# Kernel optimization log

Hardware: AMD Instinct MI355X
Metric: run time of the kernel (lower is better)

## Reference

```python
import jax, jax.numpy as jnp
import numpy as np

DIM = 384
NH = 16
HD = DIM // NH          # 24
HID = DIM * 4           # titan/cms hidden
RD = 2 * (HD // 3 // 2) # 8 rope channels per axis (d/h/w), 3*RD == HD


def _ln(x, scale, bias):
    m = x.mean(-1, keepdims=True)
    v = ((x - m) ** 2).mean(-1, keepdims=True)
    return (x - m) * jax.lax.rsqrt(v + 1e-5) * scale + bias


def _mlp(x, w1, b1, w2, b2):
    # TitanMemory / CMS level: Linear -> GELU -> Linear (titan_layers=2)
    h = jax.nn.gelu(x @ w1 + b1, approximate=False)
    return h @ w2 + b2


def _rotate(x, pos):
    # rotate_queries_or_keys: interleaved rotary. x: [B,nh,N,d], pos: [N]
    d = x.shape[-1]
    inv_freq = 1.0 / (10000.0 ** (jnp.arange(0, d, 2, dtype=jnp.float32) / d))
    ang = pos[:, None] * inv_freq[None, :]              # [N, d/2]
    sin, cos = jnp.sin(ang), jnp.cos(ang)
    x1, x2 = x[..., 0::2], x[..., 1::2]
    y1 = x1 * cos - x2 * sin
    y2 = x1 * sin + x2 * cos
    return jnp.stack([y1, y2], axis=-1).reshape(x.shape)


def _rope3d(q, T, H, W):
    # 3D RoPE on frame tokens (action_tokens=0): time / height / width axes
    B, N, D = q.shape
    qh = q.reshape(B, N, NH, HD).transpose(0, 2, 1, 3)   # [B,nh,N,hd]
    ids = jnp.arange(T * H * W)
    tpos = (ids // (H * W)).astype(jnp.float32)
    hpos = ((ids % (H * W)) // W).astype(jnp.float32)
    wpos = (ids % W).astype(jnp.float32)
    qd = _rotate(qh[..., :RD], tpos)
    qhh = _rotate(qh[..., RD:2 * RD], hpos)
    qww = _rotate(qh[..., 2 * RD:3 * RD], wpos)
    out = jnp.concatenate([qd, qhh, qww], axis=-1)
    return out.transpose(0, 2, 1, 3).reshape(B, N, D)


def setup_inputs() -> dict:
    key = jax.random.key(0)
    ks = jax.random.split(key, 8)
    B, T, H, W = 8, 8, 16, 16
    N = T * H * W
    p = lambda k, sh: jax.random.normal(k, sh, jnp.float32) * 0.02
    return {
        "x": jax.random.normal(ks[0], (B, N, DIM), jnp.float32),
        "norm1_scale": jnp.ones((DIM,), jnp.float32),
        "norm1_bias": jnp.zeros((DIM,), jnp.float32),
        "norm2_scale": jnp.ones((DIM,), jnp.float32),
        "norm2_bias": jnp.zeros((DIM,), jnp.float32),
        "q_w": p(ks[1], (DIM, DIM)),
        # stacked Titan memories: [M_k, M_v, M_eta, M_alpha, M_memory]
        "titan_w1": p(ks[2], (5, DIM, HID)),
        "titan_b1": jnp.zeros((5, HID), jnp.float32),
        "titan_w2": p(ks[3], (5, HID, DIM)),
        "titan_b2": jnp.zeros((5, DIM), jnp.float32),
        "out_w": p(ks[4], (DIM, DIM)),
        "out_b": jnp.zeros((DIM,), jnp.float32),
        # CMS levels: [fast, medium, slow]
        "cms_w1": p(ks[5], (3, DIM, HID)),
        "cms_b1": jnp.zeros((3, HID), jnp.float32),
        "cms_w2": p(ks[6], (3, HID, DIM)),
        "cms_b2": jnp.zeros((3, DIM), jnp.float32),
        "T": T, "H": H, "W": W, "action_tokens": 0,
    }


def reference(x, norm1_scale, norm1_bias, norm2_scale, norm2_bias, q_w,
              titan_w1, titan_b1, titan_w2, titan_b2, out_w, out_b,
              cms_w1, cms_b1, cms_w2, cms_b2, T, H, W, action_tokens):
    # Phase A: self-modifying Titan (eval path: retrieval only)
    y = _ln(x, norm1_scale, norm1_bias)
    q = y @ q_w                                  # static query projection (Eq. 76)
    q = _rope3d(q, T, H, W)                      # 3D RoPE (action_tokens == 0)
    out = _mlp(q, titan_w1[4], titan_b1[4], titan_w2[4], titan_b2[4])  # M_memory(q)
    out = out @ out_w + out_b                    # out_proj
    x = x + out                                  # residual (drop_path = identity)
    # Phase B: CMS multi-frequency MLP cascade
    y = _ln(x, norm2_scale, norm2_bias)
    cms = sum(_mlp(y, cms_w1[i], cms_b1[i], cms_w2[i], cms_b2[i]) for i in range(3))
    return x + cms
```

## Files before the change

kernel.cpp:

```cpp
#include <hip/hip_runtime.h>
#include <math.h>

typedef unsigned short u16;
typedef unsigned int u32;
typedef __attribute__((ext_vector_type(8))) short short8;
typedef __attribute__((ext_vector_type(4))) float f32x4;

#define DIM 384
#define HID 1536

static __device__ __forceinline__ float bf2f(u32 b){ return __uint_as_float(b << 16); }
static __device__ __forceinline__ u16 f2bf(float f){
  u32 u = __float_as_uint(f);
  u32 r = (u + 0x7fffu + ((u >> 16) & 1u)) >> 16;
  return (u16)r;
}
static __device__ __forceinline__ float gelu_fast(float v){
  float u = v * fmaf(0.0713548162726f, v * v, 1.59576912161f);
  float e = exp2f(-1.44269504089f * u);
  return v * __builtin_amdgcn_rcpf(1.0f + e);
}
static __device__ __forceinline__ void gload_lds16(const u16* g, u16* l){
  __builtin_amdgcn_global_load_lds(
      (__attribute__((address_space(1))) void*)(void*)const_cast<u16*>(g),
      (__attribute__((address_space(3))) void*)(void*)l, 16, 0, 0);
}

__global__ __launch_bounds__(256) void ln_kernel(const float* __restrict__ x,
    const float* __restrict__ sc, const float* __restrict__ bi, u16* __restrict__ y){
  int lane = threadIdx.x & 63;
  int row = blockIdx.x * 4 + (threadIdx.x >> 6);
  const float* xr = x + (size_t)row * DIM;
  float v[6];
  float s = 0.f, sq = 0.f;
#pragma unroll
  for (int i = 0; i < 6; ++i){
    float f = xr[lane + 64*i];
    v[i] = f; s += f; sq += f*f;
  }
#pragma unroll
  for (int o = 1; o < 64; o <<= 1){ s += __shfl_xor(s, o); sq += __shfl_xor(sq, o); }
  float mean = s * (1.0f/DIM);
  float var = sq * (1.0f/DIM) - mean*mean;
  float inv = rsqrtf(var + 1e-5f);
  u16* yr = y + (size_t)row * DIM;
#pragma unroll
  for (int i = 0; i < 6; ++i){
    int c = lane + 64*i;
    yr[c] = f2bf((v[i] - mean) * inv * sc[c] + bi[c]);
  }
}

__global__ __launch_bounds__(256) void rope_kernel(u16* __restrict__ q,
    const int* __restrict__ Tp, const int* __restrict__ Hp, const int* __restrict__ Wp,
    int Mtok){
  int idx = blockIdx.x * 256 + threadIdx.x;
  int tok = idx / 192;
  if (tok >= Mtok) return;
  int p = idx - tok * 192;
  int H = *Hp, W = *Wp, T = *Tp;
  int HW = H * W;
  int Ns = T * HW;
  int n = tok % Ns;
  int head = p / 12;
  int pp = p - head * 12;
  int s = pp >> 2, f = pp & 3;
  float pos;
  if (s == 0)      pos = (float)(n / HW);
  else if (s == 1) pos = (float)((n / W) % H);
  else             pos = (float)(n % W);
  const float LOG2_10000 = 13.28771237954945f;
  float inv = exp2f(-0.25f * (float)f * LOG2_10000);
  float ang = pos * inv;
  float sn = sinf(ang), cs = cosf(ang);
  size_t base = (size_t)tok * DIM + head * 24 + s * 8 + 2 * f;
  u32 u = *(u32*)(q + base);
  float x1 = bf2f(u & 0xffffu), x2 = bf2f(u >> 16);
  float y1 = x1 * cs - x2 * sn;
  float y2 = x1 * sn + x2 * cs;
  *(u32*)(q + base) = (u32)f2bf(y1) | ((u32)f2bf(y2) << 16);
}

template<int R, int C>
__global__ __launch_bounds__(256) void transpose_kernel(
    const float* __restrict__ s0, const float* __restrict__ s1,
    const float* __restrict__ s2, const float* __restrict__ s3,
    u16* __restrict__ d0, u16* __restrict__ d1, u16* __restrict__ d2, u16* __restrict__ d3,
    int dstStride){
  const float* src = (blockIdx.z == 0) ? s0 : (blockIdx.z == 1) ? s1 : (blockIdx.z == 2) ? s2 : s3;
  u16* dst         = (blockIdx.z == 0) ? d0 : (blockIdx.z == 1) ? d1 : (blockIdx.z == 2) ? d2 : d3;
  __shared__ u16 t[32][33];
  int tx = threadIdx.x & 31, ty = threadIdx.x >> 5;
  int r0 = blockIdx.y * 32, c0 = blockIdx.x * 32;
#pragma unroll
  for (int i = 0; i < 4; ++i)
    t[ty + 8*i][tx] = f2bf(src[(size_t)(r0 + ty + 8*i) * C + c0 + tx]);
  __syncthreads();
#pragma unroll
  for (int i = 0; i < 4; ++i)
    dst[(size_t)(c0 + ty + 8*i) * dstStride + r0 + tx] = t[tx][ty + 8*i];
}

__global__ void bias3_kernel(const float* __restrict__ b, float* __restrict__ o){
  int n = threadIdx.x;
  o[n] = b[n] + b[384 + n] + b[768 + n];
}

enum { E_NONE = 0, E_BIAS = 1, E_BIAS_GELU = 2, E_RES_F32 = 3, E_ACC_F32 = 4, E_FINAL = 5 };

template<int BM, int N, int K, int EPI>
__global__ __launch_bounds__(256) void gemm_kernel(
    const u16* __restrict__ A, const u16* __restrict__ Bt,
    void* __restrict__ Cv, const float* __restrict__ bias,
    const float* __restrict__ res, float* __restrict__ accbuf){
  constexpr int BN = 128, BK = 64;
  constexpr int MT = BM / 32, NT = 4;
  constexpr int AIT = BM / 32, BIT = 4;
  __shared__ __align__(16) u16 As[BM * BK];
  __shared__ __align__(16) u16 Bs[BN * BK];
  const int tid = threadIdx.x;
  const int lane = tid & 63;
  const int wv = tid >> 6;
  const int wm = (wv >> 1) * (BM / 2);
  const int wn = (wv & 1) * 64;
  const int quad = lane >> 4;
  const int l16 = lane & 15;
  const int rsw = l16 & 7;
  const size_t m0 = (size_t)blockIdx.x * BM;
  const int n0 = blockIdx.y * BN;
  const int srow = lane >> 3;
  const int scol = ((lane & 7) ^ srow) * 8;

  f32x4 acc[MT][NT];
  const f32x4 zero = {0.f, 0.f, 0.f, 0.f};
#pragma unroll
  for (int mt = 0; mt < MT; ++mt)
#pragma unroll
    for (int nt = 0; nt < NT; ++nt) acc[mt][nt] = zero;

  for (int kt = 0; kt < K; kt += BK){
#pragma unroll
    for (int i = 0; i < AIT; ++i){
      int seg = i * 4 + wv;
      gload_lds16(A + (m0 + (size_t)(seg * 8 + srow)) * K + kt + scol, As + seg * 512);
    }
#pragma unroll
    for (int i = 0; i < BIT; ++i){
      int seg = i * 4 + wv;
      gload_lds16(Bt + (size_t)(n0 + seg * 8 + srow) * K + kt + scol, Bs + seg * 512);
    }
    __syncthreads();
#pragma unroll
    for (int kk = 0; kk < 2; ++kk){
      short8 af[MT], bfr[NT];
#pragma unroll
      for (int mt = 0; mt < MT; ++mt)
        af[mt] = *(const short8*)(As + (wm + mt*16 + l16) * BK + (((kk*4 + quad) ^ rsw) << 3));
#pragma unroll
      for (int nt = 0; nt < NT; ++nt)
        bfr[nt] = *(const short8*)(Bs + (wn + nt*16 + l16) * BK + (((kk*4 + quad) ^ rsw) << 3));
#pragma unroll
      for (int mt = 0; mt < MT; ++mt)
#pragma unroll
        for (int nt = 0; nt < NT; ++nt)
          acc[mt][nt] = __builtin_amdgcn_mfma_f32_16x16x32_bf16(af[mt], bfr[nt], acc[mt][nt], 0, 0, 0);
    }
    __syncthreads();
  }

#pragma unroll
  for (int mt = 0; mt < MT; ++mt){
#pragma unroll
    for (int nt = 0; nt < NT; ++nt){
      int ncol = n0 + wn + nt*16 + l16;
      float bv = (EPI != E_NONE) ? bias[ncol] : 0.f;
      size_t mbase = m0 + wm + mt*16 + quad*4;
#pragma unroll
      for (int r = 0; r < 4; ++r){
        size_t off = (mbase + r) * N + ncol;
        float vv = acc[mt][nt][r];
        if      (EPI == E_NONE)      ((u16*)Cv)[off] = f2bf(vv);
        else if (EPI == E_BIAS)      ((u16*)Cv)[off] = f2bf(vv + bv);
        else if (EPI == E_BIAS_GELU) ((u16*)Cv)[off] = f2bf(gelu_fast(vv + bv));
        else if (EPI == E_RES_F32)   accbuf[off] = vv + bv + res[off];
        else if (EPI == E_ACC_F32)   accbuf[off] += vv + bv;
        else            ((float*)Cv)[off] = accbuf[off] + vv + bv;
      }
    }
  }
}

extern "C" void kernel_launch(void* const* d_in, const int* in_sizes, int n_in,
                              void* d_out, int out_size, void* d_ws, size_t ws_size,
                              hipStream_t stream) {
  const int W11 = DIM * HID;
  const float* x   = (const float*)d_in[0];
  const float* n1s = (const float*)d_in[1];
  const float* n1b = (const float*)d_in[2];
  const float* n2s = (const float*)d_in[3];
  const float* n2b = (const float*)d_in[4];
  const float* qw  = (const float*)d_in[5];
  const float* tw1 = (const float*)d_in[6] + 4 * W11;
  const float* tb1 = (const float*)d_in[7] + 4 * HID;
  const float* tw2 = (const float*)d_in[8] + 4 * W11;
  const float* tb2 = (const float*)d_in[9] + 4 * DIM;
  const float* ow  = (const float*)d_in[10];
  const float* ob  = (const float*)d_in[11];
  const float* cw1 = (const float*)d_in[12];
  const float* cb1 = (const float*)d_in[13];
  const float* cw2 = (const float*)d_in[14];
  const float* cb2 = (const float*)d_in[15];
  const int* Tp = (const int*)d_in[16];
  const int* Hp = (const int*)d_in[17];
  const int* Wp = (const int*)d_in[18];
  const int M = in_sizes[0] / DIM;
  const bool fused = (ws_size >= 198772224u);

  char* ws = (char*)d_ws;
  u16 *y, *h, *qwT, *owT, *w1T, *w2T, *cw1T, *cw2T;
  float *x2, *cb2s = nullptr;
  u16* qb = (u16*)d_out;
  if (fused){
    y    = (u16*) (ws + 0);
    h    = (u16*) (ws + 12582912);
    x2   = (float*)(ws + 163577856);
    qwT  = (u16*) (ws + 188743680);
    owT  = (u16*) (ws + 189038592);
    w1T  = (u16*) (ws + 189333504);
    w2T  = (u16*) (ws + 190513152);
    cw1T = (u16*) (ws + 191692800);
    cw2T = (u16*) (ws + 195231744);
    cb2s = (float*)(ws + 198770688);
  } else {
    if (ws_size < 98107392u) return;
    y    = (u16*) (ws + 0);
    h    = (u16*) (ws + 12582912);
    x2   = (float*)(ws + 62914560);
    qwT  = (u16*) (ws + 88080384);
    owT  = (u16*) (ws + 88375296);
    w1T  = (u16*) (ws + 88670208);
    w2T  = (u16*) (ws + 89849856);
    cw1T = (u16*) (ws + 91029504);
    cw2T = (u16*) (ws + 94568448);
  }

  transpose_kernel<384,384><<<dim3(12,12,2),256,0,stream>>>(
      qw, ow, qw, qw, qwT, owT, qwT, qwT, 384);
  transpose_kernel<384,1536><<<dim3(48,12,4),256,0,stream>>>(
      tw1, cw1, cw1 + W11, cw1 + 2*W11, w1T, cw1T, cw1T + W11, cw1T + 2*W11, 384);
  if (fused){
    transpose_kernel<1536,384><<<dim3(12,48,1),256,0,stream>>>(
        tw2, tw2, tw2, tw2, w2T, w2T, w2T, w2T, 1536);
    transpose_kernel<1536,384><<<dim3(12,48,3),256,0,stream>>>(
        cw2, cw2 + W11, cw2 + 2*W11, cw2, cw2T, cw2T + 1536, cw2T + 3072, cw2T, 4608);
    bias3_kernel<<<1,384,0,stream>>>(cb2, cb2s);
  } else {
    transpose_kernel<1536,384><<<dim3(12,48,4),256,0,stream>>>(
        tw2, cw2, cw2 + W11, cw2 + 2*W11, w2T, cw2T, cw2T + W11, cw2T + 2*W11, 1536);
  }

  ln_kernel<<<M/4,256,0,stream>>>(x, n1s, n1b, y);
  gemm_kernel<64,384,384,E_NONE><<<dim3(M/64,3),256,0,stream>>>(y, qwT, qb, nullptr, nullptr, nullptr);
  rope_kernel<<<(M*192)/256,256,0,stream>>>(qb, Tp, Hp, Wp, M);
  gemm_kernel<128,1536,384,E_BIAS_GELU><<<dim3(M/128,12),256,0,stream>>>(qb, w1T, h, tb1, nullptr, nullptr);
  gemm_kernel<64,384,1536,E_BIAS><<<dim3(M/64,3),256,0,stream>>>(h, w2T, qb, tb2, nullptr, nullptr);
  gemm_kernel<64,384,384,E_RES_F32><<<dim3(M/64,3),256,0,stream>>>(qb, owT, nullptr, ob, x, x2);
  ln_kernel<<<M/4,256,0,stream>>>(x2, n2s, n2b, y);
  if (fused){
    gemm_kernel<128,4608,384,E_BIAS_GELU><<<dim3(M/128,36),256,0,stream>>>(
        y, cw1T, h, cb1, nullptr, nullptr);
    gemm_kernel<64,384,4608,E_FINAL><<<dim3(M/64,3),256,0,stream>>>(
        h, cw2T, d_out, cb2s, nullptr, x2);
  } else {
    for (int i = 0; i < 3; ++i){
      gemm_kernel<128,1536,384,E_BIAS_GELU><<<dim3(M/128,12),256,0,stream>>>(
          y, cw1T + i*W11, h, cb1 + i*HID, nullptr, nullptr);
      if (i < 2)
        gemm_kernel<64,384,1536,E_ACC_F32><<<dim3(M/64,3),256,0,stream>>>(
            h, cw2T + i*W11, nullptr, cb2 + i*DIM, nullptr, x2);
      else
        gemm_kernel<64,384,1536,E_FINAL><<<dim3(M/64,3),256,0,stream>>>(
            h, cw2T + i*W11, d_out, cb2 + i*DIM, nullptr, x2);
    }
  }
}
```

Measured before the change: 434.3 us.

## Fuse MLP up-projection, GELU and down-projection into one LDS-resident kernel

Adds a fused MLP kernel in which each 64-row block keeps its input tile in LDS and loops over 128-wide hidden chunks. For each chunk it computes the first GEMM, applies bias and GELU into LDS, then accumulates the second GEMM into registers. Weight tiles are double-buffered through LDS with global_load_lds. The kernel replaces the separate GEMM pairs for both the Titan memory MLP and the concatenated CMS cascade, so the large hidden activation is never written to global memory. In exchange it uses 128KB of LDS and many accumulator registers per block, and the grid shrinks to M/64 blocks (1024), which lowers occupancy and parallelism.

Measured after the change: 1.085 ms. +149.8%, slower.

```diff
diff --git a/kernel.cpp b/kernel.cpp
--- a/kernel.cpp
+++ b/kernel.cpp
@@ -190,6 +190,154 @@
   }
 }
 
+template<int HIDN, int EPI>
+__global__ __launch_bounds__(256) void fused_mlp_kernel(
+    const u16* __restrict__ A, const u16* __restrict__ W1T,
+    const float* __restrict__ b1, const u16* __restrict__ W2T,
+    const float* __restrict__ b2, void* __restrict__ out,
+    const float* __restrict__ x2){
+  constexpr int NJ = HIDN / 128;
+  __shared__ __align__(16) u16 lds[65536];
+  u16* Ys  = lds;
+  u16* Hs  = lds + 24576;
+  u16* Wst = lds + 32768;
+
+  const int tid  = threadIdx.x;
+  const int lane = tid & 63;
+  const int wv   = tid >> 6;
+  const int mh   = (wv & 1) * 32;
+  const int wc   = wv >> 1;
+  const int quad = lane >> 4;
+  const int l16  = lane & 15;
+  const int rsw8 = l16 & 7;
+  const size_t m0 = (size_t)blockIdx.x * 64;
+
+  auto stage16 = [&](const u16* base, int S, u16* buf){
+    int rin = lane >> 4;
+    int c   = lane & 15;
+#pragma unroll
+    for (int i = 0; i < 8; ++i){
+      int seg = i * 4 + wv;
+      int row = seg * 4 + rin;
+      gload_lds16(base + (size_t)row * S + (((c ^ (row & 15)) << 3)), buf + seg * 512);
+    }
+  };
+
+  f32x4 acc2[2][12], acc1[2][4];
+  const f32x4 zero = {0.f, 0.f, 0.f, 0.f};
+#pragma unroll
+  for (int mt = 0; mt < 2; ++mt){
+#pragma unroll
+    for (int t = 0; t < 12; ++t) acc2[mt][t] = zero;
+#pragma unroll
+    for (int t = 0; t < 4; ++t)  acc1[mt][t] = zero;
+  }
+
+  {
+    int sr = lane >> 3;
+    int sc = ((lane & 7) ^ sr) * 8;
+#pragma unroll
+    for (int g = 0; g < 12; ++g){
+      int id = g * 4 + wv;
+      int s = id >> 3, seg = id & 7;
+      gload_lds16(A + (m0 + seg * 8 + sr) * 384 + s * 64 + sc, Ys + s * 4096 + seg * 512);
+    }
+  }
+  stage16(W1T, 384, Wst);
+  __syncthreads();
+
+  int pb = 0;
+#pragma unroll 1
+  for (int j = 0; j < NJ; ++j){
+#pragma unroll 1
+    for (int u = 0; u < 3; ++u){
+      if (u < 2) stage16(W1T + (size_t)j * 128 * 384 + (u + 1) * 128, 384, Wst + (pb ^ 1) * 16384);
+      else       stage16(W2T + (size_t)j * 128, HIDN, Wst + (pb ^ 1) * 16384);
+      const u16* Wb = Wst + pb * 16384;
+#pragma unroll
+      for (int kk = 0; kk < 4; ++kk){
+        short8 af[2], bfr[4];
+        int s = u * 2 + (kk >> 1);
+        int c8 = ((kk & 1) * 4 + quad) ^ rsw8;
+#pragma unroll
+        for (int mt = 0; mt < 2; ++mt)
+          af[mt] = *(const short8*)(Ys + s * 4096 + (mh + mt*16 + l16) * 64 + (c8 << 3));
+        int c16 = (kk * 4 + quad) ^ l16;
+#pragma unroll
+        for (int i = 0; i < 4; ++i)
+          bfr[i] = *(const short8*)(Wb + ((2*i + wc) * 16 + l16) * 128 + (c16 << 3));
+#pragma unroll
+        for (int mt = 0; mt < 2; ++mt)
+#pragma unroll
+          for (int i = 0; i < 4; ++i)
+            acc1[mt][i] = __builtin_amdgcn_mfma_f32_16x16x32_bf16(af[mt], bfr[i], acc1[mt][i], 0, 0, 0);
+      }
+      __syncthreads();
+      pb ^= 1;
+    }
+#pragma unroll
+    for (int i = 0; i < 4; ++i){
+      int nl = (2*i + wc) * 16 + l16;
+      float bv = b1[j * 128 + nl];
+#pragma unroll
+      for (int mt = 0; mt < 2; ++mt){
+#pragma unroll
+        for (int r = 0; r < 4; ++r){
+          int m = mh + mt*16 + quad*4 + r;
+          float v = gelu_fast(acc1[mt][i][r] + bv);
+          Hs[(nl >> 6) * 4096 + m * 64 + ((((nl >> 3) & 7) ^ (m & 7)) << 3) + (nl & 7)] = f2bf(v);
+        }
+        acc1[mt][i] = zero;
+      }
+    }
+    __syncthreads();
+#pragma unroll 1
+    for (int u = 3; u < 6; ++u){
+      int ds = u - 3;
+      if (u < 5)           stage16(W2T + (size_t)(ds + 1) * 128 * HIDN + (size_t)j * 128, HIDN, Wst + (pb ^ 1) * 16384);
+      else if (j + 1 < NJ) stage16(W1T + (size_t)(j + 1) * 128 * 384, 384, Wst + (pb ^ 1) * 16384);
+      const u16* Wb = Wst + pb * 16384;
+#pragma unroll
+      for (int kk = 0; kk < 4; ++kk){
+        short8 af[2], bfr[4];
+        int kh = kk >> 1;
+        int c8 = ((kk & 1) * 4 + quad) ^ rsw8;
+#pragma unroll
+        for (int mt = 0; mt < 2; ++mt)
+          af[mt] = *(const short8*)(Hs + kh * 4096 + (mh + mt*16 + l16) * 64 + (c8 << 3));
+        int c16 = (kk * 4 + quad) ^ l16;
+#pragma unroll
+        for (int i = 0; i < 4; ++i)
+          bfr[i] = *(const short8*)(Wb + ((2*i + wc) * 16 + l16) * 128 + (c16 << 3));
+#pragma unroll
+        for (int mt = 0; mt < 2; ++mt)
+#pragma unroll
+          for (int i = 0; i < 4; ++i)
+            acc2[mt][ds*4 + i] = __builtin_amdgcn_mfma_f32_16x16x32_bf16(af[mt], bfr[i], acc2[mt][ds*4 + i], 0, 0, 0);
+      }
+      __syncthreads();
+      pb ^= 1;
+    }
+  }
+
+#pragma unroll
+  for (int mt = 0; mt < 2; ++mt){
+#pragma unroll
+    for (int t = 0; t < 12; ++t){
+      int ds = t >> 2, i = t & 3;
+      int d = ds * 128 + (2*i + wc) * 16 + l16;
+      float bv = b2[d];
+#pragma unroll
+      for (int r = 0; r < 4; ++r){
+        size_t off = (m0 + mh + mt*16 + quad*4 + r) * 384 + d;
+        float v = acc2[mt][t][r] + bv;
+        if (EPI == 0) ((u16*)out)[off] = f2bf(v);
+        else          ((float*)out)[off] = x2[off] + v;
+      }
+    }
+  }
+}
+
 extern "C" void kernel_launch(void* const* d_in, const int* in_sizes, int n_in,
                               void* d_out, int out_size, void* d_ws, size_t ws_size,
                               hipStream_t stream) {
@@ -214,73 +362,35 @@
   const int* Hp = (const int*)d_in[17];
   const int* Wp = (const int*)d_in[18];
   const int M = in_sizes[0] / DIM;
-  const bool fused = (ws_size >= 198772224u);
 
   char* ws = (char*)d_ws;
-  u16 *y, *h, *qwT, *owT, *w1T, *w2T, *cw1T, *cw2T;
-  float *x2, *cb2s = nullptr;
-  u16* qb = (u16*)d_out;
-  if (fused){
-    y    = (u16*) (ws + 0);
-    h    = (u16*) (ws + 12582912);
-    x2   = (float*)(ws + 163577856);
-    qwT  = (u16*) (ws + 188743680);
-    owT  = (u16*) (ws + 189038592);
-    w1T  = (u16*) (ws + 189333504);
-    w2T  = (u16*) (ws + 190513152);
-    cw1T = (u16*) (ws + 191692800);
-    cw2T = (u16*) (ws + 195231744);
-    cb2s = (float*)(ws + 198770688);
-  } else {
-    if (ws_size < 98107392u) return;
-    y    = (u16*) (ws + 0);
-    h    = (u16*) (ws + 12582912);
-    x2   = (float*)(ws + 62914560);
-    qwT  = (u16*) (ws + 88080384);
-    owT  = (u16*) (ws + 88375296);
-    w1T  = (u16*) (ws + 88670208);
-    w2T  = (u16*) (ws + 89849856);
-    cw1T = (u16*) (ws + 91029504);
-    cw2T = (u16*) (ws + 94568448);
-  }
+  u16*  y    = (u16*) (ws + 0);
+  float* x2  = (float*)(ws + 12582912);
+  u16*  qwT  = (u16*) (ws + 37748736);
+  u16*  owT  = (u16*) (ws + 38043648);
+  u16*  w1T  = (u16*) (ws + 38338560);
+  u16*  w2T  = (u16*) (ws + 39518208);
+  u16*  cw1T = (u16*) (ws + 40697856);
+  u16*  cw2T = (u16*) (ws + 44236800);
+  float* cb2s = (float*)(ws + 47775744);
+  u16*  qb   = (u16*)d_out;
+  if (ws_size < 47777280u) return;
 
   transpose_kernel<384,384><<<dim3(12,12,2),256,0,stream>>>(
       qw, ow, qw, qw, qwT, owT, qwT, qwT, 384);
   transpose_kernel<384,1536><<<dim3(48,12,4),256,0,stream>>>(
       tw1, cw1, cw1 + W11, cw1 + 2*W11, w1T, cw1T, cw1T + W11, cw1T + 2*W11, 384);
-  if (fused){
-    transpose_kernel<1536,384><<<dim3(12,48,1),256,0,stream>>>(
-        tw2, tw2, tw2, tw2, w2T, w2T, w2T, w2T, 1536);
-    transpose_kernel<1536,384><<<dim3(12,48,3),256,0,stream>>>(
-        cw2, cw2 + W11, cw2 + 2*W11, cw2, cw2T, cw2T + 1536, cw2T + 3072, cw2T, 4608);
-    bias3_kernel<<<1,384,0,stream>>>(cb2, cb2s);
-  } else {
-    transpose_kernel<1536,384><<<dim3(12,48,4),256,0,stream>>>(
-        tw2, cw2, cw2 + W11, cw2 + 2*W11, w2T, cw2T, cw2T + W11, cw2T + 2*W11, 1536);
-  }
+  transpose_kernel<1536,384><<<dim3(12,48,1),256,0,stream>>>(
+      tw2, tw2, tw2, tw2, w2T, w2T, w2T, w2T, 1536);
+  transpose_kernel<1536,384><<<dim3(12,48,3),256,0,stream>>>(
+      cw2, cw2 + W11, cw2 + 2*W11, cw2, cw2T, cw2T + 1536, cw2T + 3072, cw2T, 4608);
+  bias3_kernel<<<1,384,0,stream>>>(cb2, cb2s);
 
   ln_kernel<<<M/4,256,0,stream>>>(x, n1s, n1b, y);
   gemm_kernel<64,384,384,E_NONE><<<dim3(M/64,3),256,0,stream>>>(y, qwT, qb, nullptr, nullptr, nullptr);
   rope_kernel<<<(M*192)/256,256,0,stream>>>(qb, Tp, Hp, Wp, M);
-  gemm_kernel<128,1536,384,E_BIAS_GELU><<<dim3(M/128,12),256,0,stream>>>(qb, w1T, h, tb1, nullptr, nullptr);
-  gemm_kernel<64,384,1536,E_BIAS><<<dim3(M/64,3),256,0,stream>>>(h, w2T, qb, tb2, nullptr, nullptr);
+  fused_mlp_kernel<1536,0><<<M/64,256,0,stream>>>(qb, w1T, tb1, w2T, tb2, qb, nullptr);
   gemm_kernel<64,384,384,E_RES_F32><<<dim3(M/64,3),256,0,stream>>>(qb, owT, nullptr, ob, x, x2);
   ln_kernel<<<M/4,256,0,stream>>>(x2, n2s, n2b, y);
-  if (fused){
-    gemm_kernel<128,4608,384,E_BIAS_GELU><<<dim3(M/128,36),256,0,stream>>>(
-        y, cw1T, h, cb1, nullptr, nullptr);
-    gemm_kernel<64,384,4608,E_FINAL><<<dim3(M/64,3),256,0,stream>>>(
-        h, cw2T, d_out, cb2s, nullptr, x2);
-  } else {
-    for (int i = 0; i < 3; ++i){
-      gemm_kernel<128,1536,384,E_BIAS_GELU><<<dim3(M/128,12),256,0,stream>>>(
-          y, cw1T + i*W11, h, cb1 + i*HID, nullptr, nullptr);
-      if (i < 2)
-        gemm_kernel<64,384,1536,E_ACC_F32><<<dim3(M/64,3),256,0,stream>>>(
-            h, cw2T + i*W11, nullptr, cb2 + i*DIM, nullptr, x2);
-      else
-        gemm_kernel<64,384,1536,E_FINAL><<<dim3(M/64,3),256,0,stream>>>(
-            h, cw2T + i*W11, d_out, cb2 + i*DIM, nullptr, x2);
-    }
-  }
-}
+  fused_mlp_kernel<4608,1><<<M/64,256,0,stream>>>(y, cw1T, cb1, cw2T, cb2s, d_out, x2);
+}
```
